# Optimization experiments

Hardware: AMD Instinct MI355X
Metric: run time of the kernel (lower is better)

Reference implementation:

```python
import jax, jax.numpy as jnp
import numpy as np

NEG_BIG = -9.0e15


def masked_mean_softmax(idx):
    # softmax over a 0/-inf mask == uniform weights over positions where idx > 0
    logits = jnp.where(idx > 0, 1.0, NEG_BIG).astype(jnp.float32)
    return jax.nn.softmax(logits, axis=1)


def setup_inputs() -> dict:
    key = jax.random.key(0)
    ks = jax.random.split(key, 8)
    N_NODES, N_EDGES, EDGE_ARITY, NODE_DEG = 100000, 50000, 32, 16
    D_IN, D_OUT, TV = 128, 128, 128
    stdv = 1.0 / np.sqrt(D_IN)
    u = lambda k, shp: jax.random.uniform(k, shp, jnp.float32, -stdv, stdv)
    return {
        "x": jax.random.normal(ks[0], (N_NODES, D_IN), jnp.float32),
        "seq": jax.random.randint(ks[1], (N_EDGES, EDGE_ARITY), 0, N_NODES),
        "useq": jax.random.randint(ks[2], (N_NODES, NODE_DEG), 0, N_EDGES),
        "TextVector": jax.random.normal(ks[3], (TV,), jnp.float32),
        "weight1": u(ks[4], (D_IN, D_OUT)),
        "weight2": u(ks[5], (D_OUT, D_OUT)),
        "weight3": u(ks[6], (TV, TV)),
    }


def reference(x, seq, useq, TextVector, weight1, weight2, weight3):
    # NOTE: the torch module overwrites TextVector with weight3[0]; dropout is
    # a no-op in eval mode and is omitted here.
    tv = weight3[0]                                   # [TV]
    dot = weight3 @ tv                                # [TV]
    cos = dot / (jnp.linalg.norm(tv) * jnp.linalg.norm(weight3, axis=1))
    inter_nw = jnp.mean(cos)                          # scalar

    xw = (x @ weight1) * inter_nw                     # [N, D_OUT]

    nor = masked_mean_softmax(seq)                    # [E, A]
    adj_with_fea = xw[seq]                            # [E, A, D_OUT] gather
    edge = jnp.einsum('eac,ea->ec', adj_with_fea, nor)
    edge = jax.nn.relu(edge)
    e1 = edge @ weight2                               # [E, D_OUT]

    u_nor = masked_mean_softmax(useq)                 # [N, K]
    edge_adj = e1[useq]                               # [N, K, D_OUT] gather
    node = jnp.einsum('nkc,nk->nc', edge_adj, u_nor)  # [N, D_OUT]
    return node
```

## Files before the change

### kernel.cpp

```cpp
#include <hip/hip_runtime.h>
#include <hip/hip_fp16.h>

#define ND 100000
#define NE 50000
#define AR 32
#define DG 16
#define D  128

typedef _Float16 half8_t __attribute__((ext_vector_type(8)));
typedef _Float16 half4_t __attribute__((ext_vector_type(4)));
typedef float    f32x4_t __attribute__((ext_vector_type(4)));

#define APAD 136

__global__ __launch_bounds__(256) void k_prep(const float* __restrict__ w1,
                                              const float* __restrict__ w2,
                                              const float* __restrict__ w3,
                                              _Float16* __restrict__ w1f,
                                              _Float16* __restrict__ w2f,
                                              float* __restrict__ inter_out) {
    if (blockIdx.x == 64) {
        __shared__ float red[128];
        int j = threadIdx.x;
        if (j < 128) {
            float dot = 0.f, sq = 0.f, sq0 = 0.f;
            #pragma unroll 8
            for (int k = 0; k < D; ++k) {
                float wj = w3[j * D + k];
                float w0 = w3[k];
                dot += wj * w0;
                sq  += wj * wj;
                sq0 += w0 * w0;
            }
            red[j] = dot / (sqrtf(sq0) * sqrtf(sq));
        }
        __syncthreads();
        if (j == 0) {
            float s = 0.f;
            for (int i = 0; i < 128; ++i) s += red[i];
            inter_out[0] = s / 128.f;
        }
        return;
    }
    int o = blockIdx.x * 256 + threadIdx.x;
    int j    = o & 7;
    int lane = (o >> 3) & 63;
    int frag = o >> 9;
    int ntile = frag >> 2, ktile = frag & 3;
    int n = ntile * 16 + (lane & 15);
    int k = ktile * 32 + (lane >> 4) * 8 + j;
    w1f[o] = (_Float16)w1[k * D + n];
    w2f[o] = (_Float16)w2[k * D + n];
}

__global__ __launch_bounds__(256) void k_xw(const float* __restrict__ x,
                                            const _Float16* __restrict__ w1f_g,
                                            const float* __restrict__ inter_p,
                                            _Float16* __restrict__ xwh) {
    __shared__ _Float16 wfrag[D * D];
    __shared__ _Float16 xs[64 * APAD];
    int t = threadIdx.x;
    {
        const float4* src = (const float4*)w1f_g;
        float4* dst = (float4*)wfrag;
        #pragma unroll
        for (int i = 0; i < 8; ++i) dst[i * 256 + t] = src[i * 256 + t];
    }
    int rowbase = blockIdx.x * 64;
    #pragma unroll
    for (int p = 0; p < 8; ++p) {
        int idx = p * 1024 + t * 4;
        int r = idx >> 7, c = idx & 127;
        int grow = rowbase + r;
        float4 v = make_float4(0.f, 0.f, 0.f, 0.f);
        if (grow < ND) v = ((const float4*)x)[(size_t)grow * 32 + (c >> 2)];
        half4_t h = { (_Float16)v.x, (_Float16)v.y, (_Float16)v.z, (_Float16)v.w };
        *(half4_t*)&xs[r * APAD + c] = h;
    }
    __syncthreads();

    int wave = t >> 6, lane = t & 63;
    int quad = lane >> 4, l15 = lane & 15;
    int m0 = wave * 16;
    float inter = inter_p[0];

    half8_t a[4];
    #pragma unroll
    for (int kt = 0; kt < 4; ++kt)
        a[kt] = *(const half8_t*)&xs[(m0 + l15) * APAD + kt * 32 + quad * 8];

    int grow = rowbase + m0 + l15;
    #pragma unroll
    for (int nt = 0; nt < 8; ++nt) {
        f32x4_t acc = {0.f, 0.f, 0.f, 0.f};
        #pragma unroll
        for (int kt = 0; kt < 4; ++kt) {
            half8_t b = *(const half8_t*)&wfrag[((nt * 4 + kt) * 64 + lane) * 8];
            acc = __builtin_amdgcn_mfma_f32_16x16x32_f16(b, a[kt], acc, 0, 0, 0);
        }
        half4_t hv = { (_Float16)(acc[0] * inter), (_Float16)(acc[1] * inter),
                       (_Float16)(acc[2] * inter), (_Float16)(acc[3] * inter) };
        if (grow < ND)
            *(half4_t*)(xwh + (size_t)grow * D + nt * 16 + quad * 4) = hv;
    }
}

__global__ __launch_bounds__(256) void k_gather_e(const int* __restrict__ seq,
                                                  const _Float16* __restrict__ xwh,
                                                  _Float16* __restrict__ ea) {
    int t = threadIdx.x;
    int wave = t >> 6, lane = t & 63;
    int e = lane >> 4, l16 = lane & 15;
    int le = wave * 4 + e;
    int eg = blockIdx.x * 16 + le;
    int base = e * 16;

    int sv0 = seq[(size_t)eg * AR + l16];
    int sv1 = seq[(size_t)eg * AR + 16 + l16];
    unsigned long long b0 = __ballot(sv0 > 0);
    unsigned long long b1 = __ballot(sv1 > 0);
    unsigned int f0 = (unsigned int)(b0 >> base) & 0xFFFFu;
    unsigned int f1 = (unsigned int)(b1 >> base) & 0xFFFFu;
    int cnt = __popc(f0) + __popc(f1);
    bool allv = (cnt == 0);
    if (allv) cnt = AR;
    float wv = 1.f / (float)cnt;

    float acc[8] = {};
    int colOff = l16 * 8;
    #pragma unroll
    for (int h = 0; h < 2; ++h) {
        int sreg = h ? sv1 : sv0;
        float w[16];
        const _Float16* addr[16];
        #pragma unroll
        for (int u = 0; u < 16; ++u) {
            int rr = __shfl(sreg, base + u, 64);
            w[u] = ((rr > 0) | allv) ? wv : 0.f;
            addr[u] = xwh + (size_t)rr * D + colOff;
        }
        half8_t v[16];
        #pragma unroll
        for (int u = 0; u < 16; ++u) v[u] = *(const half8_t*)addr[u];
        #pragma unroll
        for (int u = 0; u < 16; ++u) {
            #pragma unroll
            for (int jj = 0; jj < 8; ++jj)
                acc[jj] = fmaf(w[u], (float)v[u][jj], acc[jj]);
        }
    }
    half8_t hv;
    #pragma unroll
    for (int jj = 0; jj < 8; ++jj) hv[jj] = (_Float16)fmaxf(acc[jj], 0.f);
    *(half8_t*)(ea + (size_t)eg * D + colOff) = hv;
}

__global__ __launch_bounds__(256) void k_gemm_e(const _Float16* __restrict__ ea,
                                                const _Float16* __restrict__ w2f_g,
                                                _Float16* __restrict__ e1h) {
    __shared__ _Float16 wfrag[D * D];
    __shared__ _Float16 et[64 * APAD];
    int t = threadIdx.x;
    {
        const float4* src = (const float4*)w2f_g;
        float4* dst = (float4*)wfrag;
        #pragma unroll
        for (int i = 0; i < 8; ++i) dst[i * 256 + t] = src[i * 256 + t];
    }
    int rowbase = blockIdx.x * 64;
    #pragma unroll
    for (int p = 0; p < 4; ++p) {
        int hidx = p * 2048 + t * 8;
        int r = hidx >> 7, c = hidx & 127;
        int grow = rowbase + r;
        int gs = (grow < NE) ? grow : (NE - 1);
        half8_t v = *(const half8_t*)(ea + (size_t)gs * D + c);
        *(half8_t*)&et[r * APAD + c] = v;
    }
    __syncthreads();

    int wave = t >> 6, lane = t & 63;
    int quad = lane >> 4, l15 = lane & 15;
    int m0 = wave * 16;

    half8_t a[4];
    #pragma unroll
    for (int kt = 0; kt < 4; ++kt)
        a[kt] = *(const half8_t*)&et[(m0 + l15) * APAD + kt * 32 + quad * 8];

    int grow = rowbase + m0 + l15;
    #pragma unroll
    for (int nt = 0; nt < 8; ++nt) {
        f32x4_t acc = {0.f, 0.f, 0.f, 0.f};
        #pragma unroll
        for (int kt = 0; kt < 4; ++kt) {
            half8_t b = *(const half8_t*)&wfrag[((nt * 4 + kt) * 64 + lane) * 8];
            acc = __builtin_amdgcn_mfma_f32_16x16x32_f16(b, a[kt], acc, 0, 0, 0);
        }
        half4_t hv = { (_Float16)acc[0], (_Float16)acc[1],
                       (_Float16)acc[2], (_Float16)acc[3] };
        if (grow < NE)
            *(half4_t*)(e1h + (size_t)grow * D + nt * 16 + quad * 4) = hv;
    }
}

__global__ __launch_bounds__(256) void k_gather_n(const int* __restrict__ useq,
                                                  const _Float16* __restrict__ e1h,
                                                  float* __restrict__ out) {
    int t = threadIdx.x;
    int wave = t >> 6, lane = t & 63;
    int nd = lane >> 4, l16 = lane & 15;
    int ln = wave * 4 + nd;
    int ng = blockIdx.x * 16 + ln;
    int base = nd * 16;

    int sval = useq[(size_t)ng * DG + l16];
    unsigned long long b = __ballot(sval > 0);
    unsigned int f = (unsigned int)(b >> base) & 0xFFFFu;
    int cnt = __popc(f);
    bool allv = (cnt == 0);
    if (allv) cnt = DG;
    float wv = 1.f / (float)cnt;

    int colOff = l16 * 8;
    float w[16];
    const _Float16* addr[16];
    #pragma unroll
    for (int u = 0; u < 16; ++u) {
        int rr = __shfl(sval, base + u, 64);
        w[u] = ((rr > 0) | allv) ? wv : 0.f;
        addr[u] = e1h + (size_t)rr * D + colOff;
    }
    half8_t v[16];
    #pragma unroll
    for (int u = 0; u < 16; ++u) v[u] = *(const half8_t*)addr[u];

    float acc[8] = {};
    #pragma unroll
    for (int u = 0; u < 16; ++u) {
        #pragma unroll
        for (int jj = 0; jj < 8; ++jj)
            acc[jj] = fmaf(w[u], (float)v[u][jj], acc[jj]);
    }
    f32x4_t o0 = { acc[0], acc[1], acc[2], acc[3] };
    f32x4_t o1 = { acc[4], acc[5], acc[6], acc[7] };
    f32x4_t* p = (f32x4_t*)(out + (size_t)ng * D + colOff);
    __builtin_nontemporal_store(o0, p);
    __builtin_nontemporal_store(o1, p + 1);
}

extern "C" void kernel_launch(void* const* d_in, const int* in_sizes, int n_in,
                              void* d_out, int out_size, void* d_ws, size_t ws_size,
                              hipStream_t stream) {
    const float* x    = (const float*)d_in[0];
    const int*   seq  = (const int*)d_in[1];
    const int*   useq = (const int*)d_in[2];
    const float* w1   = (const float*)d_in[4];
    const float* w2   = (const float*)d_in[5];
    const float* w3   = (const float*)d_in[6];
    float* out = (float*)d_out;

    _Float16* xwh   = (_Float16*)d_out;
    _Float16* ea    = (_Float16*)d_out + (size_t)ND * D;
    float*    inter = (float*)d_ws;
    _Float16* w1f   = (_Float16*)((char*)d_ws + 256);
    _Float16* w2f   = (_Float16*)((char*)d_ws + 256 + 32768);
    _Float16* e1h   = (_Float16*)((char*)d_ws + 256 + 65536);

    hipLaunchKernelGGL(k_prep,     dim3(65),             dim3(256), 0, stream, w1, w2, w3, w1f, w2f, inter);
    hipLaunchKernelGGL(k_xw,       dim3((ND + 63) / 64), dim3(256), 0, stream, x, w1f, inter, xwh);
    hipLaunchKernelGGL(k_gather_e, dim3(NE / 16),        dim3(256), 0, stream, seq, xwh, ea);
    hipLaunchKernelGGL(k_gemm_e,   dim3((NE + 63) / 64), dim3(256), 0, stream, ea, w2f, e1h);
    hipLaunchKernelGGL(k_gather_n, dim3(ND / 16),        dim3(256), 0, stream, useq, e1h, out);
}
```

Before: 232.1 us.

## Column-slice xw and e1 tables so gathers hit cache-resident slabs

The xw and e1 intermediates are stored in column-sliced layouts: 8 slabs of 16 halfs for xw and 4 slabs of 32 halfs for e1. Each gather block now handles one slab, indexed by blockIdx low bits. The intent is that concurrent blocks touch only a few MB of table, which should fit better in L2/MALL and cut random-gather DRAM traffic. Index weights are precomputed once per block into LDS. In exchange, seq/useq are re-read per slab, each gather load is narrower (16 bytes per row segment), and there are more blocks with an added LDS stage.

```diff
diff --git a/kernel.cpp b/kernel.cpp
--- a/kernel.cpp
+++ b/kernel.cpp
@@ -12,6 +12,7 @@
 typedef float    f32x4_t __attribute__((ext_vector_type(4)));
 
 #define APAD 136
+#define EPB 128
 
 __global__ __launch_bounds__(256) void k_prep(const float* __restrict__ w1,
                                               const float* __restrict__ w2,
@@ -56,7 +57,7 @@
 __global__ __launch_bounds__(256) void k_xw(const float* __restrict__ x,
                                             const _Float16* __restrict__ w1f_g,
                                             const float* __restrict__ inter_p,
-                                            _Float16* __restrict__ xwh) {
+                                            _Float16* __restrict__ xws) {
     __shared__ _Float16 wfrag[D * D];
     __shared__ _Float16 xs[64 * APAD];
     int t = threadIdx.x;
@@ -101,63 +102,67 @@
         half4_t hv = { (_Float16)(acc[0] * inter), (_Float16)(acc[1] * inter),
                        (_Float16)(acc[2] * inter), (_Float16)(acc[3] * inter) };
         if (grow < ND)
-            *(half4_t*)(xwh + (size_t)grow * D + nt * 16 + quad * 4) = hv;
+            *(half4_t*)(xws + ((size_t)nt * ND + grow) * 16 + quad * 4) = hv;
     }
 }
 
 __global__ __launch_bounds__(256) void k_gather_e(const int* __restrict__ seq,
-                                                  const _Float16* __restrict__ xwh,
+                                                  const _Float16* __restrict__ xws,
                                                   _Float16* __restrict__ ea) {
-    int t = threadIdx.x;
-    int wave = t >> 6, lane = t & 63;
-    int e = lane >> 4, l16 = lane & 15;
-    int le = wave * 4 + e;
-    int eg = blockIdx.x * 16 + le;
-    int base = e * 16;
-
-    int sv0 = seq[(size_t)eg * AR + l16];
-    int sv1 = seq[(size_t)eg * AR + 16 + l16];
-    unsigned long long b0 = __ballot(sv0 > 0);
-    unsigned long long b1 = __ballot(sv1 > 0);
-    unsigned int f0 = (unsigned int)(b0 >> base) & 0xFFFFu;
-    unsigned int f1 = (unsigned int)(b1 >> base) & 0xFFFFu;
-    int cnt = __popc(f0) + __popc(f1);
+    __shared__ int2 iw[EPB * AR];
+    __shared__ int  cpart[256];
+    int t = threadIdx.x;
+    int s = blockIdx.x & 7;
+    int g = blockIdx.x >> 3;
+    int eg0 = g * EPB;
+
+    int e = t >> 1, part = t & 1;
+    int egs = min(eg0 + e, NE - 1);
+    const int4* sp = (const int4*)(seq + (size_t)egs * AR + part * 16);
+    int4 a = sp[0], b = sp[1], c = sp[2], d = sp[3];
+    int idxs[16] = { a.x, a.y, a.z, a.w, b.x, b.y, b.z, b.w,
+                     c.x, c.y, c.z, c.w, d.x, d.y, d.z, d.w };
+    int pc = 0;
+    #pragma unroll
+    for (int j = 0; j < 16; ++j) pc += (idxs[j] > 0);
+    cpart[t] = pc;
+    __syncthreads();
+    int cnt = cpart[e * 2] + cpart[e * 2 + 1];
     bool allv = (cnt == 0);
-    if (allv) cnt = AR;
-    float wv = 1.f / (float)cnt;
+    float wv = 1.f / (float)(allv ? AR : cnt);
+    #pragma unroll
+    for (int j = 0; j < 16; ++j) {
+        float w = (allv | (idxs[j] > 0)) ? wv : 0.f;
+        iw[e * AR + part * 16 + j] = make_int2(idxs[j], __float_as_int(w));
+    }
+    __syncthreads();
+
+    int e2 = t >> 1;
+    int chunk = t & 1;
+    const _Float16* tab = xws + (size_t)s * ND * 16;
 
     float acc[8] = {};
-    int colOff = l16 * 8;
-    #pragma unroll
-    for (int h = 0; h < 2; ++h) {
-        int sreg = h ? sv1 : sv0;
-        float w[16];
-        const _Float16* addr[16];
-        #pragma unroll
-        for (int u = 0; u < 16; ++u) {
-            int rr = __shfl(sreg, base + u, 64);
-            w[u] = ((rr > 0) | allv) ? wv : 0.f;
-            addr[u] = xwh + (size_t)rr * D + colOff;
-        }
-        half8_t v[16];
-        #pragma unroll
-        for (int u = 0; u < 16; ++u) v[u] = *(const half8_t*)addr[u];
-        #pragma unroll
-        for (int u = 0; u < 16; ++u) {
-            #pragma unroll
-            for (int jj = 0; jj < 8; ++jj)
-                acc[jj] = fmaf(w[u], (float)v[u][jj], acc[jj]);
-        }
-    }
-    half8_t hv;
-    #pragma unroll
-    for (int jj = 0; jj < 8; ++jj) hv[jj] = (_Float16)fmaxf(acc[jj], 0.f);
-    *(half8_t*)(ea + (size_t)eg * D + colOff) = hv;
+    #pragma unroll
+    for (int tt = 0; tt < AR; ++tt) {
+        int2 p = iw[e2 * AR + tt];
+        float w = __int_as_float(p.y);
+        half8_t v = *(const half8_t*)(tab + (size_t)p.x * 16 + chunk * 8);
+        #pragma unroll
+        for (int jj = 0; jj < 8; ++jj)
+            acc[jj] = fmaf(w, (float)v[jj], acc[jj]);
+    }
+    int eg = eg0 + e2;
+    if (eg < NE) {
+        half8_t h;
+        #pragma unroll
+        for (int jj = 0; jj < 8; ++jj) h[jj] = (_Float16)fmaxf(acc[jj], 0.f);
+        *(half8_t*)(ea + (size_t)eg * D + s * 16 + chunk * 8) = h;
+    }
 }
 
 __global__ __launch_bounds__(256) void k_gemm_e(const _Float16* __restrict__ ea,
                                                 const _Float16* __restrict__ w2f_g,
-                                                _Float16* __restrict__ e1h) {
+                                                _Float16* __restrict__ e1s) {
     __shared__ _Float16 wfrag[D * D];
     __shared__ _Float16 et[64 * APAD];
     int t = threadIdx.x;
@@ -200,53 +205,60 @@
         half4_t hv = { (_Float16)acc[0], (_Float16)acc[1],
                        (_Float16)acc[2], (_Float16)acc[3] };
         if (grow < NE)
-            *(half4_t*)(e1h + (size_t)grow * D + nt * 16 + quad * 4) = hv;
+            *(half4_t*)(e1s + ((size_t)(nt >> 1) * NE + grow) * 32
+                            + (nt & 1) * 16 + quad * 4) = hv;
     }
 }
 
 __global__ __launch_bounds__(256) void k_gather_n(const int* __restrict__ useq,
-                                                  const _Float16* __restrict__ e1h,
+                                                  const _Float16* __restrict__ e1s,
                                                   float* __restrict__ out) {
-    int t = threadIdx.x;
+    __shared__ int2 iw[64 * DG];
+    __shared__ int  cpart[256];
+    int t = threadIdx.x;
+    int s = blockIdx.x & 3;
+    int g = blockIdx.x >> 2;
+    int ng0 = g * 64;
+
+    int n = t >> 2, part = t & 3;
+    int ns = min(ng0 + n, ND - 1);
+    int4 a = *(const int4*)(useq + (size_t)ns * DG + part * 4);
+    cpart[t] = (a.x > 0) + (a.y > 0) + (a.z > 0) + (a.w > 0);
+    __syncthreads();
+    int cnt = cpart[n * 4] + cpart[n * 4 + 1] + cpart[n * 4 + 2] + cpart[n * 4 + 3];
+    bool allv = (cnt == 0);
+    float wv = 1.f / (float)(allv ? DG : cnt);
+    int idxs[4] = { a.x, a.y, a.z, a.w };
+    #pragma unroll
+    for (int j = 0; j < 4; ++j) {
+        float w = (allv | (idxs[j] > 0)) ? wv : 0.f;
+        iw[n * DG + part * 4 + j] = make_int2(idxs[j], __float_as_int(w));
+    }
+    __syncthreads();
+
     int wave = t >> 6, lane = t & 63;
-    int nd = lane >> 4, l16 = lane & 15;
-    int ln = wave * 4 + nd;
-    int ng = blockIdx.x * 16 + ln;
-    int base = nd * 16;
-
-    int sval = useq[(size_t)ng * DG + l16];
-    unsigned long long b = __ballot(sval > 0);
-    unsigned int f = (unsigned int)(b >> base) & 0xFFFFu;
-    int cnt = __popc(f);
-    bool allv = (cnt == 0);
-    if (allv) cnt = DG;
-    float wv = 1.f / (float)cnt;
-
-    int colOff = l16 * 8;
-    float w[16];
-    const _Float16* addr[16];
-    #pragma unroll
-    for (int u = 0; u < 16; ++u) {
-        int rr = __shfl(sval, base + u, 64);
-        w[u] = ((rr > 0) | allv) ? wv : 0.f;
-        addr[u] = e1h + (size_t)rr * D + colOff;
-    }
-    half8_t v[16];
-    #pragma unroll
-    for (int u = 0; u < 16; ++u) v[u] = *(const half8_t*)addr[u];
+    int n2 = wave * 16 + (lane >> 2);
+    int chunk = lane & 3;
+    const _Float16* tab = e1s + (size_t)s * NE * 32;
 
     float acc[8] = {};
     #pragma unroll
-    for (int u = 0; u < 16; ++u) {
+    for (int tt = 0; tt < DG; ++tt) {
+        int2 p = iw[n2 * DG + tt];
+        float w = __int_as_float(p.y);
+        half8_t v = *(const half8_t*)(tab + (size_t)p.x * 32 + chunk * 8);
         #pragma unroll
         for (int jj = 0; jj < 8; ++jj)
-            acc[jj] = fmaf(w[u], (float)v[u][jj], acc[jj]);
-    }
-    f32x4_t o0 = { acc[0], acc[1], acc[2], acc[3] };
-    f32x4_t o1 = { acc[4], acc[5], acc[6], acc[7] };
-    f32x4_t* p = (f32x4_t*)(out + (size_t)ng * D + colOff);
-    __builtin_nontemporal_store(o0, p);
-    __builtin_nontemporal_store(o1, p + 1);
+            acc[jj] = fmaf(w, (float)v[jj], acc[jj]);
+    }
+    int ng = ng0 + n2;
+    if (ng < ND) {
+        f32x4_t o0 = { acc[0], acc[1], acc[2], acc[3] };
+        f32x4_t o1 = { acc[4], acc[5], acc[6], acc[7] };
+        f32x4_t* p = (f32x4_t*)(out + (size_t)ng * D + s * 32 + chunk * 8);
+        __builtin_nontemporal_store(o0, p);
+        __builtin_nontemporal_store(o1, p + 1);
+    }
 }
 
 extern "C" void kernel_launch(void* const* d_in, const int* in_sizes, int n_in,
@@ -260,16 +272,19 @@
     const float* w3   = (const float*)d_in[6];
     float* out = (float*)d_out;
 
-    _Float16* xwh   = (_Float16*)d_out;
+    _Float16* xws   = (_Float16*)d_out;
     _Float16* ea    = (_Float16*)d_out + (size_t)ND * D;
     float*    inter = (float*)d_ws;
     _Float16* w1f   = (_Float16*)((char*)d_ws + 256);
     _Float16* w2f   = (_Float16*)((char*)d_ws + 256 + 32768);
-    _Float16* e1h   = (_Float16*)((char*)d_ws + 256 + 65536);
+    _Float16* e1s   = (_Float16*)((char*)d_ws + 256 + 65536);
+
+    int eg_grp = (NE + EPB - 1) / EPB;
+    int ng_grp = (ND + 63) / 64;
 
     hipLaunchKernelGGL(k_prep,     dim3(65),             dim3(256), 0, stream, w1, w2, w3, w1f, w2f, inter);
-    hipLaunchKernelGGL(k_xw,       dim3((ND + 63) / 64), dim3(256), 0, stream, x, w1f, inter, xwh);
-    hipLaunchKernelGGL(k_gather_e, dim3(NE / 16),        dim3(256), 0, stream, seq, xwh, ea);
-    hipLaunchKernelGGL(k_gemm_e,   dim3((NE + 63) / 64), dim3(256), 0, stream, ea, w2f, e1h);
-    hipLaunchKernelGGL(k_gather_n, dim3(ND / 16),        dim3(256), 0, stream, useq, e1h, out);
-}
+    hipLaunchKernelGGL(k_xw,       dim3((ND + 63) / 64), dim3(256), 0, stream, x, w1f, inter, xws);
+    hipLaunchKernelGGL(k_gather_e, dim3(eg_grp * 8),     dim3(256), 0, stream, seq, xws, ea);
+    hipLaunchKernelGGL(k_gemm_e,   dim3((NE + 63) / 64), dim3(256), 0, stream, ea, w2f, e1s);
+    hipLaunchKernelGGL(k_gather_n, dim3(ng_grp * 4),     dim3(256), 0, stream, useq, e1s, out);
+}
```

Measured after the change: 227.5 us. 1.02x faster.
